# Optimization experiments

Measured on AMD Instinct MI355X. Metric: run time of the kernel, lower is better.

The kernel has to match this reference:

```python
import jax, jax.numpy as jnp
import numpy as np

B, L, D, H = 4, 2048, 1024, 16
DH = D // H
SCALE = DH ** -0.5


def setup_inputs() -> dict:
    key = jax.random.key(0)
    ks = jax.random.split(key, 8)
    q = jax.random.normal(ks[0], (B, L, D), dtype=jnp.float32)
    k = jax.random.normal(ks[1], (B, L, D), dtype=jnp.float32)
    v = jax.random.normal(ks[2], (B, L, D), dtype=jnp.float32)
    mask = jax.random.randint(ks[3], (B, 1, L), 0, 2, dtype=jnp.int32)
    s = D ** -0.5
    Wq = jax.random.normal(ks[4], (D, D), dtype=jnp.float32) * s
    Wk = jax.random.normal(ks[5], (D, D), dtype=jnp.float32) * s
    Wv = jax.random.normal(ks[6], (D, D), dtype=jnp.float32) * s
    Wo = jax.random.normal(ks[7], (D, D), dtype=jnp.float32) * s
    return {"q": q, "k": k, "v": v, "mask": mask, "Wq": Wq, "Wk": Wk, "Wv": Wv, "Wo": Wo}


def reference(q, k, v, mask, Wq, Wk, Wv, Wo):
    b, l, d = q.shape
    # torch Linear (no bias): x @ W^T; split heads -> [B, H, T, DH]
    qh = (q @ Wq.T).reshape(b, l, H, DH).transpose(0, 2, 1, 3)
    kh = (k @ Wk.T).reshape(b, -1, H, DH).transpose(0, 2, 1, 3)
    vh = (v @ Wv.T).reshape(b, -1, H, DH).transpose(0, 2, 1, 3)
    # scores [B, H, L, S]
    scores = jnp.einsum('bhld,bhsd->bhls', qh, kh) * SCALE
    scores = jnp.where(mask[:, None, :, :] != 1, jnp.float32(-1e9), scores)
    attn = jax.nn.softmax(scores, axis=-1)  # dropout defined but never applied in original forward
    out = jnp.einsum('bhls,bhsd->bhld', attn, vh)
    out = out.transpose(0, 2, 1, 3).reshape(b, l, d)
    return out @ Wo.T
```

## Files before the change

### kernel.cpp

```cpp
#include <hip/hip_runtime.h>
#include <cstddef>
#include <cstdint>

#define BB 4
#define LL 2048
#define DD 1024
#define HH 16
#define DHD 64
#define QSCALE 0.18033688f

typedef short s16x8 __attribute__((ext_vector_type(8)));
typedef short s16x4 __attribute__((ext_vector_type(4)));
typedef float f32x4 __attribute__((ext_vector_type(4)));
typedef unsigned int u32;
typedef u32 u32x2 __attribute__((ext_vector_type(2)));
typedef u32 u32x4 __attribute__((ext_vector_type(4)));

__device__ __forceinline__ short f2bf(float f) {
  union { float f; u32 u; } x; x.f = f;
  u32 r = x.u + 0x7FFFu + ((x.u >> 16) & 1u);
  return (short)(r >> 16);
}
__device__ __forceinline__ u32 pack2bf(float a, float b) {
  union { float f; u32 u; } x, y; x.f = a; y.f = b;
  return __builtin_amdgcn_perm(y.u + 0x8000u, x.u + 0x8000u, 0x07060302u);
}
__device__ __forceinline__ u32 cvtpk2bf(float lo, float hi) {
  u32 r;
  asm("v_cvt_pk_bf16_f32 %0, %1, %2" : "=v"(r) : "v"(lo), "v"(hi));
  return r;
}
__device__ __forceinline__ void gl2lds16(const short* g, short* l) {
  __builtin_amdgcn_global_load_lds(
      (const __attribute__((address_space(1))) unsigned int*)g,
      (__attribute__((address_space(3))) unsigned int*)l, 16, 0, 0);
}

__global__ __launch_bounds__(256) void prep_kernel(const float* __restrict__ q,
                                                   const float* __restrict__ k,
                                                   const float* __restrict__ v,
                                                   const float* __restrict__ Wq,
                                                   const float* __restrict__ Wk,
                                                   const float* __restrict__ Wv,
                                                   const float* __restrict__ Wo,
                                                   const int* __restrict__ mask,
                                                   short* __restrict__ qb,
                                                   short* __restrict__ kb,
                                                   short* __restrict__ vb,
                                                   short* __restrict__ Wqb,
                                                   short* __restrict__ Wkb,
                                                   short* __restrict__ Wvb,
                                                   short* __restrict__ Wob,
                                                   float* __restrict__ maskadd) {
  const int bb = blockIdx.x;
  if (bb < 24576) {
    const float* s; short* d;
    const int y = bb >> 13;
    if (y == 0) { s = q; d = qb; }
    else if (y == 1) { s = k; d = kb; }
    else { s = v; d = vb; }
    int i = (bb & 8191) * 256 + threadIdx.x;
    float4 x = ((const float4*)s)[i];
    s16x4 o; o.x = f2bf(x.x); o.y = f2bf(x.y); o.z = f2bf(x.z); o.w = f2bf(x.w);
    ((s16x4*)d)[i] = o;
  } else if (bb < 28672) {
    const int y = (bb - 24576) >> 10;
    const float* s; short* d; float sc = 1.0f;
    if (y == 0) { s = Wq; d = Wqb; sc = QSCALE; }
    else if (y == 1) { s = Wk; d = Wkb; }
    else if (y == 2) { s = Wv; d = Wvb; }
    else { s = Wo; d = Wob; }
    int i = ((bb - 24576) & 1023) * 256 + threadIdx.x;
    float4 x = ((const float4*)s)[i];
    s16x4 o; o.x = f2bf(x.x * sc); o.y = f2bf(x.y * sc); o.z = f2bf(x.z * sc); o.w = f2bf(x.w * sc);
    ((s16x4*)d)[i] = o;
  } else {
    int i = (bb - 28672) * 256 + threadIdx.x;
    int4 m = ((const int4*)mask)[i];
    f32x4 o;
    o[0] = (m.x == 1) ? 0.0f : -30000.0f;
    o[1] = (m.y == 1) ? 0.0f : -30000.0f;
    o[2] = (m.z == 1) ? 0.0f : -30000.0f;
    o[3] = (m.w == 1) ? 0.0f : -30000.0f;
    ((f32x4*)maskadd)[i] = o;
  }
}

__device__ __forceinline__ void gemm_core(const short* __restrict__ A, const short* __restrict__ B,
                                          int K, int bm, int bn, short* As, short* Bs,
                                          f32x4 (&acc)[4][4]) {
  const int tid = threadIdx.x;
  const int lane = tid & 63, wave = tid >> 6;
  const int wv = __builtin_amdgcn_readfirstlane(wave);
  const int quad = lane >> 4, l16 = lane & 15;
  const int wm = (wave >> 1) * 64, wn = (wave & 1) * 64;
  const short* ap[4]; const short* bp[4]; short* la[4]; short* lb[4];
#pragma unroll
  for (int t = 0; t < 4; ++t) {
    int s = wv * 256 + t * 64 + lane;
    int r = s >> 3, gl = (s & 7) ^ (r & 7);
    ap[t] = A + (size_t)(bm + r) * K + gl * 8;
    bp[t] = B + (size_t)(bn + r) * K + gl * 8;
    la[t] = &As[(wv * 256 + t * 64) * 8];
    lb[t] = &Bs[(wv * 256 + t * 64) * 8];
  }
  const int sw0 = (quad ^ (l16 & 7)) * 8;
  const int sw1 = ((4 + quad) ^ (l16 & 7)) * 8;
  for (int kk = 0; kk < K; kk += 64) {
    __syncthreads();
#pragma unroll
    for (int t = 0; t < 4; ++t) gl2lds16(ap[t] + kk, la[t]);
#pragma unroll
    for (int t = 0; t < 4; ++t) gl2lds16(bp[t] + kk, lb[t]);
    __syncthreads();
#pragma unroll
    for (int c = 0; c < 2; ++c) {
      const int sw = c ? sw1 : sw0;
      s16x8 af[4], bf[4];
#pragma unroll
      for (int t = 0; t < 4; ++t) af[t] = *(const s16x8*)&As[(wm + t * 16 + l16) * 64 + sw];
#pragma unroll
      for (int t = 0; t < 4; ++t) bf[t] = *(const s16x8*)&Bs[(wn + t * 16 + l16) * 64 + sw];
      __builtin_amdgcn_s_setprio(1);
#pragma unroll
      for (int mt = 0; mt < 4; ++mt)
#pragma unroll
        for (int nt = 0; nt < 4; ++nt)
          acc[mt][nt] = __builtin_amdgcn_mfma_f32_16x16x32_bf16(af[mt], bf[nt], acc[mt][nt], 0, 0, 0);
      __builtin_amdgcn_s_setprio(0);
    }
  }
}

__global__ __launch_bounds__(256) void qkv_gemm(const short* __restrict__ qb, const short* __restrict__ kb,
                                                const short* __restrict__ vb, const short* __restrict__ Wqb,
                                                const short* __restrict__ Wkb, const short* __restrict__ Wvb,
                                                short* __restrict__ Qh, short* __restrict__ Kh,
                                                short* __restrict__ VT) {
  __shared__ short As[128 * 64];
  __shared__ short Bs[128 * 64];
  const int bid = blockIdx.x + ((blockIdx.y + (blockIdx.z << 6)) << 3);
  const int swz = (bid & 7) * 192 + (bid >> 3);
  const int bx = swz & 7, by = (swz >> 3) & 63, z = swz >> 9;
  const short *A, *B; short* C;
  if (z == 0) { A = qb; B = Wqb; C = Qh; }
  else if (z == 1) { A = kb; B = Wkb; C = Kh; }
  else { A = Wvb; B = vb; C = VT; }
  const int bm = (z == 2 ? bx : by) * 128;
  const int bn = (z == 2 ? by : bx) * 128;
  f32x4 acc[4][4] = {};
  gemm_core(A, B, DD, bm, bn, As, Bs, acc);

  const int lane = threadIdx.x & 63, wave = threadIdx.x >> 6;
  const int quad = lane >> 4, l16 = lane & 15;
  const int wm = (wave >> 1) * 64, wn = (wave & 1) * 64;
#pragma unroll
  for (int mt = 0; mt < 4; ++mt)
#pragma unroll
    for (int nt = 0; nt < 4; ++nt)
#pragma unroll
      for (int i = 0; i < 4; ++i) {
        int m = bm + wm + mt * 16 + quad * 4 + i;
        int n = bn + wn + nt * 16 + l16;
        float val = acc[mt][nt][i];
        if (z < 2) {
          int b = m >> 11, l = m & 2047;
          C[((size_t)(b * HH + (n >> 6)) << 17) + (size_t)l * DHD + (n & 63)] = f2bf(val);
        } else {
          int b = n >> 11, l = n & 2047;
          int loc = l & 63;
          int p = (loc & 0x23) | ((loc & 0x0C) << 1) | ((loc & 0x10) >> 2);
          C[((size_t)(b * DD + m) << 11) + (l & ~63) + p] = f2bf(val);
        }
      }
}

__global__ __launch_bounds__(256) void out_gemm(const short* __restrict__ A, const short* __restrict__ B,
                                                float* __restrict__ C) {
  __shared__ short As[128 * 64];
  __shared__ short Bs[128 * 64];
  const int bid = blockIdx.x + (blockIdx.y << 3);
  const int swz = (bid & 7) * 64 + (bid >> 3);
  const int bx = swz & 7, by = swz >> 3;
  const int bm = by * 128, bn = bx * 128;
  f32x4 acc[4][4] = {};
  gemm_core(A, B, DD, bm, bn, As, Bs, acc);
  const int lane = threadIdx.x & 63, wave = threadIdx.x >> 6;
  const int quad = lane >> 4, l16 = lane & 15;
  const int wm = (wave >> 1) * 64, wn = (wave & 1) * 64;
#pragma unroll
  for (int mt = 0; mt < 4; ++mt)
#pragma unroll
    for (int nt = 0; nt < 4; ++nt)
#pragma unroll
      for (int i = 0; i < 4; ++i) {
        int m = bm + wm + mt * 16 + quad * 4 + i;
        int n = bn + wn + nt * 16 + l16;
        C[(size_t)m * DD + n] = acc[mt][nt][i];
      }
}

__global__ __launch_bounds__(256, 4) void attn_kernel(const short* __restrict__ Qh,
                                                      const short* __restrict__ Kh,
                                                      const short* __restrict__ VT,
                                                      const float* __restrict__ maskadd,
                                                      short* __restrict__ AO) {
  __shared__ short Ks[2][64 * 64];
  __shared__ short Vs[2][64 * 64];
  const int tid  = threadIdx.x;
  const int lane = tid & 63, wave = tid >> 6;
  const int wv   = __builtin_amdgcn_readfirstlane(wave);
  const int quad = lane >> 4, l16 = lane & 15;
  const int a7 = l16 & 7;

  const int bid = blockIdx.x + (blockIdx.y << 4);
  const int swz = (bid & 7) * 128 + (bid >> 3);
  const int bx = swz & 15, bh = swz >> 4;
  const int b = bh >> 4;
  const int q0 = bx * 128;

  const float* mrow = maskadd + b * LL;
  const short* Qb = Qh + (size_t)bh * LL * DHD;
  const short* Kb = Kh + (size_t)bh * LL * DHD;
  const short* Vb = VT + (size_t)bh * DHD * LL;

  s16x8 qf[2][2];
#pragma unroll
  for (int u = 0; u < 2; ++u)
#pragma unroll
    for (int c = 0; c < 2; ++c)
      qf[u][c] = *(const s16x8*)&Qb[(size_t)(q0 + wv * 32 + u * 16 + l16) * DHD + c * 32 + quad * 8];

  const short* kp[2]; const short* vp[2]; int off[2];
#pragma unroll
  for (int t = 0; t < 2; ++t) {
    int s = wv * 128 + t * 64 + lane;
    int r = s >> 3, gl = (s & 7) ^ (r & 7);
    kp[t] = Kb + (size_t)r * DHD + gl * 8;
    vp[t] = Vb + (size_t)r * LL + gl * 8;
    off[t] = (wv * 128 + t * 64) * 8;
  }
  const int sw0 = (quad ^ a7) * 8;
  const int sw1 = ((4 + quad) ^ a7) * 8;

  s16x8 vone;
#pragma unroll
  for (int j = 0; j < 8; ++j) vone[j] = (short)0x3F80;

  f32x4 lsum[2] = {};
  f32x4 accO[2][4] = {};

#pragma unroll
  for (int t = 0; t < 2; ++t) gl2lds16(kp[t], &Ks[0][off[t]]);
#pragma unroll
  for (int t = 0; t < 2; ++t) gl2lds16(vp[t], &Vs[0][off[t]]);

  int cur = 0;
  for (int s0 = 0; s0 < LL; s0 += 64) {
    __syncthreads();
    if (s0 + 64 < LL) {
#pragma unroll
      for (int t = 0; t < 2; ++t) gl2lds16(kp[t] + (size_t)(s0 + 64) * DHD, &Ks[cur ^ 1][off[t]]);
#pragma unroll
      for (int t = 0; t < 2; ++t) gl2lds16(vp[t] + (s0 + 64), &Vs[cur ^ 1][off[t]]);
    }
    f32x4 mm[4];
#pragma unroll
    for (int st = 0; st < 4; ++st) mm[st] = *(const f32x4*)&mrow[s0 + st * 16 + quad * 4];

    const short* Kc = Ks[cur];
    const short* Vc = Vs[cur];
    s16x8 kf[4][2];
#pragma unroll
    for (int st = 0; st < 4; ++st) {
      kf[st][0] = *(const s16x8*)&Kc[(st * 16 + l16) * 64 + sw0];
      kf[st][1] = *(const s16x8*)&Kc[(st * 16 + l16) * 64 + sw1];
    }
    f32x4 sc[2][4];
#pragma unroll
    for (int u = 0; u < 2; ++u)
#pragma unroll
      for (int st = 0; st < 4; ++st) {
        sc[u][st] = __builtin_amdgcn_mfma_f32_16x16x32_bf16(kf[st][0], qf[u][0], mm[st], 0, 0, 0);
        sc[u][st] = __builtin_amdgcn_mfma_f32_16x16x32_bf16(kf[st][1], qf[u][1], sc[u][st], 0, 0, 0);
      }

    s16x8 pf[2][2];
#pragma unroll
    for (int u = 0; u < 2; ++u)
#pragma unroll
      for (int c = 0; c < 2; ++c) {
        union { u32x4 u4; s16x8 s8; } cv;
#pragma unroll
        for (int h = 0; h < 2; ++h) {
          const int st = 2 * c + h;
          float p0 = __builtin_amdgcn_exp2f(sc[u][st][0]);
          float p1 = __builtin_amdgcn_exp2f(sc[u][st][1]);
          float p2 = __builtin_amdgcn_exp2f(sc[u][st][2]);
          float p3 = __builtin_amdgcn_exp2f(sc[u][st][3]);
          cv.u4[h * 2 + 0] = cvtpk2bf(p0, p1);
          cv.u4[h * 2 + 1] = cvtpk2bf(p2, p3);
        }
        pf[u][c] = cv.s8;
      }

#pragma unroll
    for (int u = 0; u < 2; ++u) {
      lsum[u] = __builtin_amdgcn_mfma_f32_16x16x32_bf16(pf[u][0], vone, lsum[u], 0, 0, 0);
      lsum[u] = __builtin_amdgcn_mfma_f32_16x16x32_bf16(pf[u][1], vone, lsum[u], 0, 0, 0);
    }
#pragma unroll
    for (int dt = 0; dt < 4; ++dt) {
      const int drow = (dt * 16 + l16) * 64;
#pragma unroll
      for (int c = 0; c < 2; ++c) {
        s16x8 vf = *(const s16x8*)&Vc[drow + (((c * 4 + quad) ^ a7) << 3)];
#pragma unroll
        for (int u = 0; u < 2; ++u)
          accO[u][dt] = __builtin_amdgcn_mfma_f32_16x16x32_bf16(pf[u][c], vf, accO[u][dt], 0, 0, 0);
      }
    }
    cur ^= 1;
  }

  short* AOb = AO + (size_t)b * LL * DD + (size_t)(bh & 15) * DHD;
#pragma unroll
  for (int u = 0; u < 2; ++u) {
    f32x4 rl;
#pragma unroll
    for (int i = 0; i < 4; ++i) rl[i] = __builtin_amdgcn_rcpf(lsum[u][i]);
#pragma unroll
    for (int dt = 0; dt < 4; ++dt)
#pragma unroll
      for (int i = 0; i < 4; ++i) {
        int qr = q0 + wv * 32 + u * 16 + quad * 4 + i;
        AOb[(size_t)qr * DD + dt * 16 + l16] = f2bf(accO[u][dt][i] * rl[i]);
      }
  }
}

extern "C" void kernel_launch(void* const* d_in, const int* in_sizes, int n_in,
                              void* d_out, int out_size, void* d_ws, size_t ws_size,
                              hipStream_t stream) {
  const float* q   = (const float*)d_in[0];
  const float* k   = (const float*)d_in[1];
  const float* v   = (const float*)d_in[2];
  const int*  mask = (const int*)d_in[3];
  const float* Wq  = (const float*)d_in[4];
  const float* Wk  = (const float*)d_in[5];
  const float* Wv  = (const float*)d_in[6];
  const float* Wo  = (const float*)d_in[7];

  const size_t SX = (size_t)BB * LL * DD;
  const size_t SW = (size_t)DD * DD;
  short* w = (short*)d_ws;
  short* qb  = w;        short* kb  = qb + SX;  short* vb  = kb + SX;
  short* Wqb = vb + SX;  short* Wkb = Wqb + SW; short* Wvb = Wkb + SW; short* Wob = Wvb + SW;
  short* Qh  = Wob + SW; short* Kh  = Qh + SX;  short* VT  = Kh + SX;
  float* maskadd = (float*)(VT + SX);
  short* AO = qb;

  prep_kernel<<<28680, 256, 0, stream>>>(q, k, v, Wq, Wk, Wv, Wo, mask,
                                         qb, kb, vb, Wqb, Wkb, Wvb, Wob, maskadd);
  qkv_gemm<<<dim3(8, 64, 3), 256, 0, stream>>>(qb, kb, vb, Wqb, Wkb, Wvb, Qh, Kh, VT);
  attn_kernel<<<dim3(LL / 128, BB * HH), 256, 0, stream>>>(Qh, Kh, VT, maskadd, AO);
  out_gemm<<<dim3(8, 64), 256, 0, stream>>>(AO, Wob, (float*)d_out);
}
```

Measured before the change: 312.0 us.

## Double-buffer GEMM LDS tiles with K=32 steps and prefetch next tile

```diff
diff --git a/kernel.cpp b/kernel.cpp
--- a/kernel.cpp
+++ b/kernel.cpp
@@ -94,41 +94,47 @@
   const int wv = __builtin_amdgcn_readfirstlane(wave);
   const int quad = lane >> 4, l16 = lane & 15;
   const int wm = (wave >> 1) * 64, wn = (wave & 1) * 64;
-  const short* ap[4]; const short* bp[4]; short* la[4]; short* lb[4];
-#pragma unroll
-  for (int t = 0; t < 4; ++t) {
-    int s = wv * 256 + t * 64 + lane;
-    int r = s >> 3, gl = (s & 7) ^ (r & 7);
-    ap[t] = A + (size_t)(bm + r) * K + gl * 8;
-    bp[t] = B + (size_t)(bn + r) * K + gl * 8;
-    la[t] = &As[(wv * 256 + t * 64) * 8];
-    lb[t] = &Bs[(wv * 256 + t * 64) * 8];
-  }
-  const int sw0 = (quad ^ (l16 & 7)) * 8;
-  const int sw1 = ((4 + quad) ^ (l16 & 7)) * 8;
-  for (int kk = 0; kk < K; kk += 64) {
+  const short* ap[2]; const short* bp[2]; int lofs[2];
+#pragma unroll
+  for (int i = 0; i < 2; ++i) {
+    int s = wv * 128 + i * 64 + lane;
+    int r = s >> 2, c = s & 3;
+    ap[i] = A + (size_t)(bm + r) * K + c * 8;
+    bp[i] = B + (size_t)(bn + r) * K + c * 8;
+    lofs[i] = s * 8;
+  }
+  const int rd = quad << 3;
+
+#pragma unroll
+  for (int i = 0; i < 2; ++i) gl2lds16(ap[i], &As[lofs[i]]);
+#pragma unroll
+  for (int i = 0; i < 2; ++i) gl2lds16(bp[i], &Bs[lofs[i]]);
+
+  int cur = 0;
+  for (int kk = 0; kk < K; kk += 32) {
     __syncthreads();
-#pragma unroll
-    for (int t = 0; t < 4; ++t) gl2lds16(ap[t] + kk, la[t]);
-#pragma unroll
-    for (int t = 0; t < 4; ++t) gl2lds16(bp[t] + kk, lb[t]);
-    __syncthreads();
-#pragma unroll
-    for (int c = 0; c < 2; ++c) {
-      const int sw = c ? sw1 : sw0;
-      s16x8 af[4], bf[4];
-#pragma unroll
-      for (int t = 0; t < 4; ++t) af[t] = *(const s16x8*)&As[(wm + t * 16 + l16) * 64 + sw];
-#pragma unroll
-      for (int t = 0; t < 4; ++t) bf[t] = *(const s16x8*)&Bs[(wn + t * 16 + l16) * 64 + sw];
-      __builtin_amdgcn_s_setprio(1);
-#pragma unroll
-      for (int mt = 0; mt < 4; ++mt)
-#pragma unroll
-        for (int nt = 0; nt < 4; ++nt)
-          acc[mt][nt] = __builtin_amdgcn_mfma_f32_16x16x32_bf16(af[mt], bf[nt], acc[mt][nt], 0, 0, 0);
-      __builtin_amdgcn_s_setprio(0);
-    }
+    if (kk + 32 < K) {
+      const int nb = (cur ^ 1) * (128 * 32);
+#pragma unroll
+      for (int i = 0; i < 2; ++i) gl2lds16(ap[i] + kk + 32, &As[nb + lofs[i]]);
+#pragma unroll
+      for (int i = 0; i < 2; ++i) gl2lds16(bp[i] + kk + 32, &Bs[nb + lofs[i]]);
+    }
+    const short* Ac = &As[cur * (128 * 32)];
+    const short* Bc = &Bs[cur * (128 * 32)];
+    s16x8 af[4], bf[4];
+#pragma unroll
+    for (int t = 0; t < 4; ++t) af[t] = *(const s16x8*)&Ac[(wm + t * 16 + l16) * 32 + rd];
+#pragma unroll
+    for (int t = 0; t < 4; ++t) bf[t] = *(const s16x8*)&Bc[(wn + t * 16 + l16) * 32 + rd];
+    __builtin_amdgcn_s_setprio(1);
+#pragma unroll
+    for (int mt = 0; mt < 4; ++mt)
+#pragma unroll
+      for (int nt = 0; nt < 4; ++nt)
+        acc[mt][nt] = __builtin_amdgcn_mfma_f32_16x16x32_bf16(af[mt], bf[nt], acc[mt][nt], 0, 0, 0);
+    __builtin_amdgcn_s_setprio(0);
+    cur ^= 1;
   }
 }
 
@@ -137,8 +143,8 @@
                                                 const short* __restrict__ Wkb, const short* __restrict__ Wvb,
                                                 short* __restrict__ Qh, short* __restrict__ Kh,
                                                 short* __restrict__ VT) {
-  __shared__ short As[128 * 64];
-  __shared__ short Bs[128 * 64];
+  __shared__ short As[2 * 128 * 32];
+  __shared__ short Bs[2 * 128 * 32];
   const int bid = blockIdx.x + ((blockIdx.y + (blockIdx.z << 6)) << 3);
   const int swz = (bid & 7) * 192 + (bid >> 3);
   const int bx = swz & 7, by = (swz >> 3) & 63, z = swz >> 9;
@@ -177,8 +183,8 @@
 
 __global__ __launch_bounds__(256) void out_gemm(const short* __restrict__ A, const short* __restrict__ B,
                                                 float* __restrict__ C) {
-  __shared__ short As[128 * 64];
-  __shared__ short Bs[128 * 64];
+  __shared__ short As[2 * 128 * 32];
+  __shared__ short Bs[2 * 128 * 32];
   const int bid = blockIdx.x + (blockIdx.y << 3);
   const int swz = (bid & 7) * 64 + (bid >> 3);
   const int bx = swz & 7, by = swz >> 3;
```

After: 308.7 us. No clear change (-1.0%).
